# Optimization experiments

Measured on AMD Instinct MI355X. Metric: run time of the kernel, lower is better.

The kernel has to match this reference:

```python
import jax, jax.numpy as jnp
import numpy as np

NUM_HEADS = 16
DIM = 1024
B, L = 2, 2048
NEG = -10000000000.0


def setup_inputs() -> dict:
    key = jax.random.key(0)
    ks = jax.random.split(key, 8)
    queries = jax.random.normal(ks[0], (B, L, DIM), dtype=jnp.float32)
    keys = jax.random.normal(ks[1], (B, L, DIM), dtype=jnp.float32)
    values = jax.random.normal(ks[2], (B, L, DIM), dtype=jnp.float32)
    mask = jax.random.uniform(ks[3], (B, L, L)) < 0.1
    s = 1.0 / np.sqrt(DIM)
    Wq = jax.random.uniform(ks[4], (DIM, DIM), minval=-s, maxval=s, dtype=jnp.float32)
    Wk = jax.random.uniform(ks[5], (DIM, DIM), minval=-s, maxval=s, dtype=jnp.float32)
    Wv = jax.random.uniform(ks[6], (DIM, DIM), minval=-s, maxval=s, dtype=jnp.float32)
    Wo = jax.random.uniform(ks[7], (DIM, DIM), minval=-s, maxval=s, dtype=jnp.float32)
    return {"queries": queries, "keys": keys, "values": values, "mask": mask,
            "Wq": Wq, "Wk": Wk, "Wv": Wv, "Wo": Wo}


def reference(queries, keys, values, mask, Wq, Wk, Wv, Wo):
    b, l, d = queries.shape
    h = NUM_HEADS
    dk = d // h
    # torch Linear(bias=False): y = x @ W.T ; then view(b, l, dk, h) -> head axis LAST
    qs = (queries @ Wq.T).reshape(b, l, dk, h)
    ks = (keys @ Wk.T).reshape(b, l, dk, h)
    vs = (values @ Wv.T).reshape(b, l, dk, h)
    # routing is None in the live code path
    w = jnp.einsum('bidh,bodh->bioh', qs, ks) / jnp.sqrt(jnp.asarray(dk, jnp.float32))
    w = jnp.where(mask[..., None], NEG, w)          # masked_fill where mask True
    w = jax.nn.softmax(w, axis=-2)                   # softmax over key axis 'o'
    mha = jnp.einsum('bioh,bodh->bidh', w, vs).reshape(b, l, d)
    # dropout is identity in eval mode
    return mha @ Wo.T
```

## Files before the change

kernel.cpp:

```cpp
#include <hip/hip_runtime.h>
#include <hip/hip_bf16.h>
#include <cstdint>
#include <cstddef>

typedef unsigned short ushort_t;
typedef __attribute__((ext_vector_type(8))) short short8;
typedef __attribute__((ext_vector_type(8))) unsigned short ushort8;
typedef __attribute__((ext_vector_type(4))) unsigned short ushort4v;
typedef __attribute__((ext_vector_type(4))) float f32x4;
typedef __attribute__((ext_vector_type(2))) unsigned long long ull2;

#define LPAD 72
#define GPAD 40
#define PSTR 40

__device__ __forceinline__ unsigned short f2bf(float f) {
    unsigned int x = __float_as_uint(f);
    unsigned int r = x + 0x7fffu + ((x >> 16) & 1u);
    return (unsigned short)(r >> 16);
}

__global__ __launch_bounds__(256) void cvt(const float* __restrict__ q,
                                           const float* __restrict__ k,
                                           const float* __restrict__ v,
                                           const float* __restrict__ Wq,
                                           const float* __restrict__ Wk,
                                           const float* __restrict__ Wv,
                                           ushort_t* __restrict__ qb,
                                           ushort_t* __restrict__ kb,
                                           ushort_t* __restrict__ vb,
                                           ushort_t* __restrict__ Wqb,
                                           ushort_t* __restrict__ Wkb,
                                           ushort_t* __restrict__ Wvb) {
    const int z = blockIdx.y;
    const float* X = (z == 0) ? q : (z == 1) ? k : v;
    const float* W = (z == 0) ? Wq : (z == 1) ? Wk : Wv;
    ushort_t* Xo = (z == 0) ? qb : (z == 1) ? kb : vb;
    ushort_t* Wo2 = (z == 0) ? Wqb : (z == 1) ? Wkb : Wvb;
    const size_t idx = (((size_t)blockIdx.x << 8) + threadIdx.x) << 3;
    const float* src; ushort_t* dst; float sc = 1.0f;
    if (idx < 4194304) { src = X + idx; dst = Xo + idx; if (z == 0) sc = 0.125f; }
    else               { src = W + (idx - 4194304); dst = Wo2 + (idx - 4194304); }
    f32x4 a0 = *(const f32x4*)src, a1 = *(const f32x4*)(src + 4);
    ushort8 o;
    #pragma unroll
    for (int j = 0; j < 4; j++) { o[j] = f2bf(a0[j] * sc); o[j + 4] = f2bf(a1[j] * sc); }
    *(ushort8*)dst = o;
}

__global__ __launch_bounds__(256) void maskbits_kernel(const int* __restrict__ mask,
                                                       unsigned long long* __restrict__ Mbits) {
    const int row  = blockIdx.x;
    const int w    = threadIdx.x >> 6;
    const int lane = threadIdx.x & 63;
    const int* mrow = mask + (size_t)row * 2048;
    #pragma unroll
    for (int it = 0; it < 8; it++) {
        const int o = (it << 8) + (w << 6) + lane;
        const unsigned long long bb = __ballot(mrow[o] != 0);
        if (lane == 0) Mbits[(size_t)((it << 2) + w) * 4096 + row] = bb;
    }
}

__global__ __launch_bounds__(256) void woswz(const float* __restrict__ W,
                                             ushort_t* __restrict__ WoH) {
    __shared__ float row[1024 + 64];
    const int j = blockIdx.x, t = threadIdx.x;
    f32x4 v = *(const f32x4*)(W + (size_t)j * 1024 + (t << 2));
    #pragma unroll
    for (int s = 0; s < 4; s++) { const int c = (t << 2) + s; row[c + (c >> 4)] = v[s]; }
    __syncthreads();
    #pragma unroll
    for (int s = 0; s < 4; s++) {
        const int k = t + (s << 8);
        const int col = ((k & 63) << 4) + (k >> 6);
        WoH[(size_t)j * 1024 + k] = f2bf(row[col + (col >> 4)]);
    }
}

__global__ __launch_bounds__(256) void gemm_proj(const ushort_t* __restrict__ qb,
                                                 const ushort_t* __restrict__ kb,
                                                 const ushort_t* __restrict__ vb,
                                                 const ushort_t* __restrict__ Wqb,
                                                 const ushort_t* __restrict__ Wkb,
                                                 const ushort_t* __restrict__ Wvb,
                                                 ushort_t* __restrict__ Qh,
                                                 ushort_t* __restrict__ Kh,
                                                 ushort_t* __restrict__ VhT) {
    __shared__ ushort_t smem[2 * 128 * PSTR];
    ushort_t* Xs = smem;
    ushort_t* Ws = smem + 128 * PSTR;

    const int z = blockIdx.z;
    const ushort_t* Xb = (z == 0) ? qb : (z == 1) ? kb : vb;
    const ushort_t* Wb = (z == 0) ? Wqb : (z == 1) ? Wkb : Wvb;

    const int tid  = threadIdx.x;
    const int n0   = blockIdx.x << 7;
    const int m0   = blockIdx.y << 7;
    const int w    = tid >> 6;
    const int lane = tid & 63;
    const int lm   = lane & 15;
    const int quad = lane >> 4;
    const int wm   = w & 1;
    const int wn   = w >> 1;

    f32x4 acc[4][4];
    #pragma unroll
    for (int i = 0; i < 4; i++)
        #pragma unroll
        for (int j = 0; j < 4; j++) acc[i][j] = (f32x4){0.f, 0.f, 0.f, 0.f};

    for (int k0 = 0; k0 < 1024; k0 += 32) {
        __syncthreads();
        #pragma unroll
        for (int cc = 0; cc < 2; cc++) {
            const int ch  = tid + (cc << 8);
            const int row = ch >> 2, c4 = ch & 3;
            *(ushort8*)&Xs[row * PSTR + (c4 << 3)] =
                *(const ushort8*)(Xb + (size_t)(m0 + row) * 1024 + k0 + (c4 << 3));
            *(ushort8*)&Ws[row * PSTR + (c4 << 3)] =
                *(const ushort8*)(Wb + (size_t)(n0 + row) * 1024 + k0 + (c4 << 3));
        }
        __syncthreads();
        short8 af[4], bf[4];
        #pragma unroll
        for (int mf = 0; mf < 4; mf++)
            af[mf] = *(const short8*)&Xs[((wm << 6) + (mf << 4) + lm) * PSTR + (quad << 3)];
        #pragma unroll
        for (int nf = 0; nf < 4; nf++)
            bf[nf] = *(const short8*)&Ws[((wn << 6) + (nf << 4) + lm) * PSTR + (quad << 3)];
        #pragma unroll
        for (int mf = 0; mf < 4; mf++)
            #pragma unroll
            for (int nf = 0; nf < 4; nf++)
                acc[mf][nf] = __builtin_amdgcn_mfma_f32_16x16x32_bf16(af[mf], bf[nf], acc[mf][nf], 0, 0, 0);
    }

    ushort_t* E = smem;
    const int bb = m0 >> 11;
    const int l0 = m0 & 2047;
    #pragma unroll
    for (int h0 = 0; h0 < 2; h0++) {
        __syncthreads();
        if (wn == h0) {
            #pragma unroll
            for (int mf = 0; mf < 4; mf++)
                #pragma unroll
                for (int nf = 0; nf < 4; nf++)
                    #pragma unroll
                    for (int r = 0; r < 4; r++) {
                        const int row = (wm << 6) + (mf << 4) + (quad << 2) + r;
                        const unsigned short val = f2bf(acc[mf][nf][r]);
                        if (z != 2) E[(lm << 9) + (row << 2) + nf] = val;
                        else        E[(lm << 9) + (nf << 7) + row] = val;
                    }
        }
        __syncthreads();
        const int dbase = (n0 + (h0 << 6)) >> 4;
        if (z != 2) {
            ushort_t* OUT = (z == 0) ? Qh : Kh;
            #pragma unroll
            for (int s = 0; s < 8; s++) {
                const int p = (tid << 3) + s;
                const int h = p >> 7, l = p & 127;
                *(ushort4v*)(OUT + ((size_t)((bb << 4) + h) * 2048 + l0 + l) * 64 + dbase) =
                    *(const ushort4v*)&E[(h << 9) + (l << 2)];
            }
        } else {
            #pragma unroll
            for (int s = 0; s < 4; s++) {
                const int p = (tid << 2) + s;
                const int h = p >> 6, nf = (p >> 4) & 3, lc = p & 15;
                *(ushort8*)(VhT + (((size_t)((bb << 4) + h) << 6) + dbase + nf) * 2048 + l0 + (lc << 3)) =
                    *(const ushort8*)&E[(h << 9) + (nf << 7) + (lc << 3)];
            }
        }
    }
}

__global__ __launch_bounds__(256) void gemm_out(const ushort_t* __restrict__ mhaH,
                                                const ushort_t* __restrict__ WoH,
                                                float* __restrict__ C) {
    __shared__ ushort_t Xs[64][GPAD];
    __shared__ ushort_t Ws[64][GPAD];
    const int tid  = threadIdx.x;
    const int m0   = blockIdx.y << 6;
    const int n0   = blockIdx.x << 6;
    const int w    = tid >> 6;
    const int lane = tid & 63;
    const int lm   = lane & 15;
    const int quad = lane >> 4;
    const int srow = tid >> 2;
    const int skc  = (tid & 3) << 3;

    f32x4 acc[4] = {{0.f,0.f,0.f,0.f},{0.f,0.f,0.f,0.f},{0.f,0.f,0.f,0.f},{0.f,0.f,0.f,0.f}};

    const int arow = m0 + srow;
    const int ab = arow >> 11, al = arow & 2047;

    for (int k0 = 0; k0 < 1024; k0 += 32) {
        const int h  = k0 >> 6;
        const int d0 = k0 & 63;
        __syncthreads();
        *(ushort8*)&Xs[srow][skc] =
            *(const ushort8*)(mhaH + ((((size_t)(ab * 16 + h)) * 2048 + al) << 6) + d0 + skc);
        *(ushort8*)&Ws[srow][skc] =
            *(const ushort8*)(WoH + (size_t)(n0 + srow) * 1024 + k0 + skc);
        __syncthreads();
        short8 af = *(const short8*)&Xs[(w << 4) + lm][quad << 3];
        #pragma unroll
        for (int c = 0; c < 4; c++) {
            short8 bf = *(const short8*)&Ws[(c << 4) + lm][quad << 3];
            acc[c] = __builtin_amdgcn_mfma_f32_16x16x32_bf16(af, bf, acc[c], 0, 0, 0);
        }
    }
    #pragma unroll
    for (int c = 0; c < 4; c++) {
        #pragma unroll
        for (int r = 0; r < 4; r++) {
            const int row = m0 + (w << 4) + (quad << 2) + r;
            const int col = n0 + (c << 4) + lm;
            C[(size_t)row * 1024 + col] = acc[c][r];
        }
    }
}

__global__ __launch_bounds__(256, 2) void flash_attn(const ushort_t* __restrict__ Qh,
                                                     const ushort_t* __restrict__ Kh,
                                                     const ushort_t* __restrict__ VhT,
                                                     const unsigned long long* __restrict__ Mbits,
                                                     ushort_t* __restrict__ mhaH) {
    __shared__ ushort_t Ks[64 * LPAD];
    __shared__ ushort_t Vt[64 * LPAD];
    __shared__ ushort_t Pw[4][16 * LPAD];

    const int tid  = threadIdx.x;
    const int w    = tid >> 6;
    const int lane = tid & 63;
    const int lm   = lane & 15;
    const int quad = lane >> 4;
    const int bh   = blockIdx.y;
    const int b    = bh >> 4;
    const int q0   = blockIdx.x << 7;

    const ushort_t* Qb  = Qh  + ((size_t)bh << 17);
    const ushort_t* Kb  = Kh  + ((size_t)bh << 17);
    const ushort_t* Vtb = VhT + ((size_t)bh << 17);

    short8 aq[2][2];
    #pragma unroll
    for (int g = 0; g < 2; g++) {
        const ushort_t* qp = Qb + (size_t)(q0 + (w << 5) + (g << 4) + lm) * 64 + (quad << 3);
        aq[g][0] = *(const short8*)qp;
        aq[g][1] = *(const short8*)(qp + 32);
    }

    float l_part[2][4] = {{0.f,0.f,0.f,0.f},{0.f,0.f,0.f,0.f}};
    f32x4 o_acc[2][4] = {{{0.f,0.f,0.f,0.f},{0.f,0.f,0.f,0.f},{0.f,0.f,0.f,0.f},{0.f,0.f,0.f,0.f}},
                         {{0.f,0.f,0.f,0.f},{0.f,0.f,0.f,0.f},{0.f,0.f,0.f,0.f},{0.f,0.f,0.f,0.f}}};

    const int chunk0  = tid << 1;
    const int rowbase = (b << 11) + q0 + (w << 5);

    for (int kt0 = 0; kt0 < 2048; kt0 += 64) {
        __syncthreads();
        #pragma unroll
        for (int cc = 0; cc < 2; cc++) {
            const int chunk = chunk0 + cc;
            const int rr = chunk >> 3;
            const int rc = (chunk & 7) << 3;
            *(ushort8*)&Ks[rr * LPAD + rc] =
                *(const ushort8*)(Kb + (size_t)(kt0 + rr) * 64 + rc);
            *(ushort8*)&Vt[rr * LPAD + rc] =
                *(const ushort8*)(Vtb + (size_t)rr * 2048 + kt0 + rc);
        }
        __syncthreads();

        short8 bk[4][2], bv[4][2];
        #pragma unroll
        for (int c = 0; c < 4; c++) {
            bk[c][0] = *(const short8*)&Ks[((c << 4) + lm) * LPAD + (quad << 3)];
            bk[c][1] = *(const short8*)&Ks[((c << 4) + lm) * LPAD + 32 + (quad << 3)];
            bv[c][0] = *(const short8*)&Vt[((c << 4) + lm) * LPAD + (quad << 3)];
            bv[c][1] = *(const short8*)&Vt[((c << 4) + lm) * LPAD + 32 + (quad << 3)];
        }

        const unsigned long long* Mt = Mbits + (size_t)(kt0 >> 6) * 4096 + rowbase;

        #pragma unroll
        for (int g = 0; g < 2; g++) {
            f32x4 s[4];
            #pragma unroll
            for (int c = 0; c < 4; c++) {
                f32x4 zz = {0.f, 0.f, 0.f, 0.f};
                zz = __builtin_amdgcn_mfma_f32_16x16x32_bf16(aq[g][0], bk[c][0], zz, 0, 0, 0);
                zz = __builtin_amdgcn_mfma_f32_16x16x32_bf16(aq[g][1], bk[c][1], zz, 0, 0, 0);
                s[c] = zz;
            }
            unsigned long long mb[4];
            {
                const unsigned long long* mp = Mt + (g << 4) + (quad << 2);
                ull2 t0 = *(const ull2*)mp;
                ull2 t1 = *(const ull2*)(mp + 2);
                mb[0] = t0[0]; mb[1] = t0[1]; mb[2] = t1[0]; mb[3] = t1[1];
            }
            #pragma unroll
            for (int r = 0; r < 4; r++) {
                const unsigned lo = (unsigned)mb[r];
                const unsigned hi = (unsigned)(mb[r] >> 32);
                float lsum = 0.f;
                #pragma unroll
                for (int c = 0; c < 4; c++) {
                    const unsigned word = (c & 2) ? hi : lo;
                    const unsigned bit = (word >> (((c & 1) << 4) + lm)) & 1u;
                    const float p = bit ? 0.f : __expf(s[c][r]);
                    s[c][r] = p;
                    lsum += p;
                }
                l_part[g][r] += lsum;
            }
            #pragma unroll
            for (int c = 0; c < 4; c++)
                #pragma unroll
                for (int r = 0; r < 4; r++)
                    Pw[w][((quad << 2) + r) * LPAD + (c << 4) + lm] = f2bf(s[c][r]);

            short8 ap0 = *(const short8*)&Pw[w][lm * LPAD + (quad << 3)];
            short8 ap1 = *(const short8*)&Pw[w][lm * LPAD + 32 + (quad << 3)];
            #pragma unroll
            for (int cd = 0; cd < 4; cd++) {
                o_acc[g][cd] = __builtin_amdgcn_mfma_f32_16x16x32_bf16(ap0, bv[cd][0], o_acc[g][cd], 0, 0, 0);
                o_acc[g][cd] = __builtin_amdgcn_mfma_f32_16x16x32_bf16(ap1, bv[cd][1], o_acc[g][cd], 0, 0, 0);
            }
        }
    }

    #pragma unroll
    for (int g = 0; g < 2; g++) {
        #pragma unroll
        for (int r = 0; r < 4; r++) {
            float l = l_part[g][r];
            l += __shfl_xor(l, 1, 64);
            l += __shfl_xor(l, 2, 64);
            l += __shfl_xor(l, 4, 64);
            l += __shfl_xor(l, 8, 64);
            const float inv_l = 1.0f / l;
            const int i = q0 + (w << 5) + (g << 4) + (quad << 2) + r;
            ushort_t* orow = mhaH + (((size_t)bh * 2048 + i) << 6);
            #pragma unroll
            for (int cd = 0; cd < 4; cd++)
                orow[(cd << 4) + lm] = f2bf(o_acc[g][cd][r] * inv_l);
        }
    }
}

extern "C" void kernel_launch(void* const* d_in, const int* in_sizes, int n_in,
                              void* d_out, int out_size, void* d_ws, size_t ws_size,
                              hipStream_t stream) {
    const float* q    = (const float*)d_in[0];
    const float* k    = (const float*)d_in[1];
    const float* v    = (const float*)d_in[2];
    const int*   mask = (const int*)d_in[3];
    const float* Wq   = (const float*)d_in[4];
    const float* Wk   = (const float*)d_in[5];
    const float* Wv   = (const float*)d_in[6];
    const float* Wo   = (const float*)d_in[7];
    float* out = (float*)d_out;

    ushort_t* qb   = (ushort_t*)d_ws;
    ushort_t* kb   = qb  + 4194304;
    ushort_t* vb   = kb  + 4194304;
    ushort_t* Wqb  = vb  + 4194304;
    ushort_t* Wkb  = Wqb + 1048576;
    ushort_t* Wvb  = Wkb + 1048576;
    ushort_t* Qh   = Wvb + 1048576;
    ushort_t* Kh   = Qh  + 4194304;
    ushort_t* VhT  = Kh  + 4194304;
    ushort_t* mhaH = qb;
    ushort_t* WoH  = kb;
    unsigned long long* Mbits = (unsigned long long*)(kb + 1048576);

    dim3 gb(256);
    cvt<<<dim3(2560, 3), gb, 0, stream>>>(q, k, v, Wq, Wk, Wv, qb, kb, vb, Wqb, Wkb, Wvb);
    gemm_proj<<<dim3(8, 32, 3), gb, 0, stream>>>(qb, kb, vb, Wqb, Wkb, Wvb, Qh, Kh, VhT);
    maskbits_kernel<<<dim3(4096), gb, 0, stream>>>(mask, Mbits);
    woswz<<<dim3(1024), gb, 0, stream>>>(Wo, WoH);
    flash_attn<<<dim3(16, 32), gb, 0, stream>>>(Qh, Kh, VhT, Mbits, mhaH);
    gemm_out<<<dim3(16, 64), gb, 0, stream>>>(mhaH, WoH, out);
}
```

Baseline: 327.2 us.

## Use direct global-to-LDS async loads in projection and output GEMMs

Replaces register-staged global→shared copies in gemm_proj and gemm_out with global_load_lds 16-byte transfers into a k-chunk-major LDS layout. The projection epilogue now writes bf16 results straight from registers instead of staging through shared memory, and the grid is flattened with a block-index remap so blocks sharing a weight tile run together. The aim is to cut VGPR staging and LDS round-trips. The unpadded layout and scattered 8-byte epilogue stores may add bank conflicts or less coalesced writes.

```diff
diff --git a/kernel.cpp b/kernel.cpp
--- a/kernel.cpp
+++ b/kernel.cpp
@@ -11,13 +11,18 @@
 typedef __attribute__((ext_vector_type(2))) unsigned long long ull2;
 
 #define LPAD 72
-#define GPAD 40
-#define PSTR 40
 
 __device__ __forceinline__ unsigned short f2bf(float f) {
     unsigned int x = __float_as_uint(f);
     unsigned int r = x + 0x7fffu + ((x >> 16) & 1u);
     return (unsigned short)(r >> 16);
+}
+
+__device__ __forceinline__ void async16(const ushort_t* g, ushort_t* l) {
+    __builtin_amdgcn_global_load_lds(
+        (const __attribute__((address_space(1))) unsigned int*)g,
+        (__attribute__((address_space(3))) unsigned int*)l,
+        16, 0, 0);
 }
 
 __global__ __launch_bounds__(256) void cvt(const float* __restrict__ q,
@@ -87,17 +92,21 @@
                                                  ushort_t* __restrict__ Qh,
                                                  ushort_t* __restrict__ Kh,
                                                  ushort_t* __restrict__ VhT) {
-    __shared__ ushort_t smem[2 * 128 * PSTR];
-    ushort_t* Xs = smem;
-    ushort_t* Ws = smem + 128 * PSTR;
-
-    const int z = blockIdx.z;
+    __shared__ ushort_t Xs[512 * 8];
+    __shared__ ushort_t Ws[512 * 8];
+
+    const int lid  = blockIdx.x;
+    const int nIdx = lid / 96;
+    const int rem  = lid % 96;
+    const int z    = rem >> 5;
+    const int mIdx = rem & 31;
+    const int n0   = nIdx << 7;
+    const int m0   = mIdx << 7;
+
     const ushort_t* Xb = (z == 0) ? qb : (z == 1) ? kb : vb;
     const ushort_t* Wb = (z == 0) ? Wqb : (z == 1) ? Wkb : Wvb;
 
     const int tid  = threadIdx.x;
-    const int n0   = blockIdx.x << 7;
-    const int m0   = blockIdx.y << 7;
     const int w    = tid >> 6;
     const int lane = tid & 63;
     const int lm   = lane & 15;
@@ -114,76 +123,60 @@
     for (int k0 = 0; k0 < 1024; k0 += 32) {
         __syncthreads();
         #pragma unroll
-        for (int cc = 0; cc < 2; cc++) {
-            const int ch  = tid + (cc << 8);
-            const int row = ch >> 2, c4 = ch & 3;
-            *(ushort8*)&Xs[row * PSTR + (c4 << 3)] =
-                *(const ushort8*)(Xb + (size_t)(m0 + row) * 1024 + k0 + (c4 << 3));
-            *(ushort8*)&Ws[row * PSTR + (c4 << 3)] =
-                *(const ushort8*)(Wb + (size_t)(n0 + row) * 1024 + k0 + (c4 << 3));
-        }
-        __syncthreads();
-        short8 af[4], bf[4];
+        for (int i = 0; i < 2; i++) {
+            const int L   = (((w << 1) + i) << 6) + lane;
+            const int c4  = L >> 7, row = L & 127;
+            const int lb  = (((w << 1) + i) << 6) << 3;
+            async16(Xb + (size_t)(m0 + row) * 1024 + k0 + (c4 << 3), &Xs[lb]);
+            async16(Wb + (size_t)(n0 + row) * 1024 + k0 + (c4 << 3), &Ws[lb]);
+        }
+        __syncthreads();
+        short8 af[4], bf4[4];
         #pragma unroll
         for (int mf = 0; mf < 4; mf++)
-            af[mf] = *(const short8*)&Xs[((wm << 6) + (mf << 4) + lm) * PSTR + (quad << 3)];
+            af[mf] = *(const short8*)&Xs[((quad << 7) + (wm << 6) + (mf << 4) + lm) << 3];
         #pragma unroll
         for (int nf = 0; nf < 4; nf++)
-            bf[nf] = *(const short8*)&Ws[((wn << 6) + (nf << 4) + lm) * PSTR + (quad << 3)];
+            bf4[nf] = *(const short8*)&Ws[((quad << 7) + (wn << 6) + (nf << 4) + lm) << 3];
         #pragma unroll
         for (int mf = 0; mf < 4; mf++)
             #pragma unroll
             for (int nf = 0; nf < 4; nf++)
-                acc[mf][nf] = __builtin_amdgcn_mfma_f32_16x16x32_bf16(af[mf], bf[nf], acc[mf][nf], 0, 0, 0);
-    }
-
-    ushort_t* E = smem;
-    const int bb = m0 >> 11;
-    const int l0 = m0 & 2047;
-    #pragma unroll
-    for (int h0 = 0; h0 < 2; h0++) {
-        __syncthreads();
-        if (wn == h0) {
-            #pragma unroll
-            for (int mf = 0; mf < 4; mf++)
-                #pragma unroll
-                for (int nf = 0; nf < 4; nf++)
-                    #pragma unroll
-                    for (int r = 0; r < 4; r++) {
-                        const int row = (wm << 6) + (mf << 4) + (quad << 2) + r;
-                        const unsigned short val = f2bf(acc[mf][nf][r]);
-                        if (z != 2) E[(lm << 9) + (row << 2) + nf] = val;
-                        else        E[(lm << 9) + (nf << 7) + row] = val;
-                    }
-        }
-        __syncthreads();
-        const int dbase = (n0 + (h0 << 6)) >> 4;
-        if (z != 2) {
-            ushort_t* OUT = (z == 0) ? Qh : Kh;
-            #pragma unroll
-            for (int s = 0; s < 8; s++) {
-                const int p = (tid << 3) + s;
-                const int h = p >> 7, l = p & 127;
-                *(ushort4v*)(OUT + ((size_t)((bb << 4) + h) * 2048 + l0 + l) * 64 + dbase) =
-                    *(const ushort4v*)&E[(h << 9) + (l << 2)];
-            }
-        } else {
-            #pragma unroll
-            for (int s = 0; s < 4; s++) {
-                const int p = (tid << 2) + s;
-                const int h = p >> 6, nf = (p >> 4) & 3, lc = p & 15;
-                *(ushort8*)(VhT + (((size_t)((bb << 4) + h) << 6) + dbase + nf) * 2048 + l0 + (lc << 3)) =
-                    *(const ushort8*)&E[(h << 9) + (nf << 7) + (lc << 3)];
-            }
-        }
+                acc[mf][nf] = __builtin_amdgcn_mfma_f32_16x16x32_bf16(af[mf], bf4[nf], acc[mf][nf], 0, 0, 0);
+    }
+
+    const int bb    = m0 >> 11;
+    const int l0    = m0 & 2047;
+    const int dbase = (n0 >> 4) + (wn << 2);
+    if (z != 2) {
+        ushort_t* OUT = (z == 0) ? Qh : Kh;
+        #pragma unroll
+        for (int mf = 0; mf < 4; mf++)
+            #pragma unroll
+            for (int r = 0; r < 4; r++) {
+                const int row = (wm << 6) + (mf << 4) + (quad << 2) + r;
+                ushort4v o = { f2bf(acc[mf][0][r]), f2bf(acc[mf][1][r]),
+                               f2bf(acc[mf][2][r]), f2bf(acc[mf][3][r]) };
+                *(ushort4v*)(OUT + ((size_t)((bb << 4) + lm) * 2048 + l0 + row) * 64 + dbase) = o;
+            }
+    } else {
+        #pragma unroll
+        for (int mf = 0; mf < 4; mf++)
+            #pragma unroll
+            for (int nf = 0; nf < 4; nf++) {
+                const int lbase = l0 + (wm << 6) + (mf << 4) + (quad << 2);
+                ushort4v o = { f2bf(acc[mf][nf][0]), f2bf(acc[mf][nf][1]),
+                               f2bf(acc[mf][nf][2]), f2bf(acc[mf][nf][3]) };
+                *(ushort4v*)(VhT + ((size_t)((bb << 4) + lm) * 64 + dbase + nf) * 2048 + lbase) = o;
+            }
     }
 }
 
 __global__ __launch_bounds__(256) void gemm_out(const ushort_t* __restrict__ mhaH,
                                                 const ushort_t* __restrict__ WoH,
                                                 float* __restrict__ C) {
-    __shared__ ushort_t Xs[64][GPAD];
-    __shared__ ushort_t Ws[64][GPAD];
+    __shared__ ushort_t Xs[256 * 8];
+    __shared__ ushort_t Ws[256 * 8];
     const int tid  = threadIdx.x;
     const int m0   = blockIdx.y << 6;
     const int n0   = blockIdx.x << 6;
@@ -191,27 +184,24 @@
     const int lane = tid & 63;
     const int lm   = lane & 15;
     const int quad = lane >> 4;
-    const int srow = tid >> 2;
-    const int skc  = (tid & 3) << 3;
+    const int ab   = m0 >> 11;
+    const int al0  = m0 & 2047;
 
     f32x4 acc[4] = {{0.f,0.f,0.f,0.f},{0.f,0.f,0.f,0.f},{0.f,0.f,0.f,0.f},{0.f,0.f,0.f,0.f}};
-
-    const int arow = m0 + srow;
-    const int ab = arow >> 11, al = arow & 2047;
 
     for (int k0 = 0; k0 < 1024; k0 += 32) {
         const int h  = k0 >> 6;
         const int d0 = k0 & 63;
         __syncthreads();
-        *(ushort8*)&Xs[srow][skc] =
-            *(const ushort8*)(mhaH + ((((size_t)(ab * 16 + h)) * 2048 + al) << 6) + d0 + skc);
-        *(ushort8*)&Ws[srow][skc] =
-            *(const ushort8*)(WoH + (size_t)(n0 + srow) * 1024 + k0 + skc);
-        __syncthreads();
-        short8 af = *(const short8*)&Xs[(w << 4) + lm][quad << 3];
+        async16(mhaH + (((size_t)(ab * 16 + h)) * 2048 + al0 + lane) * 64 + d0 + (w << 3),
+                &Xs[(w << 6) << 3]);
+        async16(WoH + (size_t)(n0 + lane) * 1024 + k0 + (w << 3),
+                &Ws[(w << 6) << 3]);
+        __syncthreads();
+        short8 af = *(const short8*)&Xs[((quad << 6) + (w << 4) + lm) << 3];
         #pragma unroll
         for (int c = 0; c < 4; c++) {
-            short8 bf = *(const short8*)&Ws[(c << 4) + lm][quad << 3];
+            short8 bf = *(const short8*)&Ws[((quad << 6) + (c << 4) + lm) << 3];
             acc[c] = __builtin_amdgcn_mfma_f32_16x16x32_bf16(af, bf, acc[c], 0, 0, 0);
         }
     }
@@ -383,7 +373,7 @@
 
     dim3 gb(256);
     cvt<<<dim3(2560, 3), gb, 0, stream>>>(q, k, v, Wq, Wk, Wv, qb, kb, vb, Wqb, Wkb, Wvb);
-    gemm_proj<<<dim3(8, 32, 3), gb, 0, stream>>>(qb, kb, vb, Wqb, Wkb, Wvb, Qh, Kh, VhT);
+    gemm_proj<<<dim3(768), gb, 0, stream>>>(qb, kb, vb, Wqb, Wkb, Wvb, Qh, Kh, VhT);
     maskbits_kernel<<<dim3(4096), gb, 0, stream>>>(mask, Mbits);
     woswz<<<dim3(1024), gb, 0, stream>>>(Wo, WoH);
     flash_attn<<<dim3(16, 32), gb, 0, stream>>>(Qh, Kh, VhT, Mbits, mhaH);
```

Measured after the change: 326.9 us. About the same (-0.1%).
